# Kernel tuning notes

Hardware: AMD Instinct MI355X
Metric: run time of the kernel (lower is better)

The kernel has to match this reference:

```python
import math
import jax, jax.numpy as jnp
import numpy as np

B, T, D = 8, 2048, 256
N_TICKS, DT, P_MIN, P_MAX = 3, 1.0, 2.0, 4.0


def setup_inputs() -> dict:
    key = jax.random.key(0)
    ks = jax.random.split(key, 16)
    s = 1.0 / math.sqrt(D)
    w = lambda k: jax.random.normal(k, (D, D), jnp.float32) * s
    zb = jnp.zeros((D,), jnp.float32)
    return {
        "z": jax.random.normal(ks[0], (B, T, D), jnp.float32),
        "in_w": w(ks[1]), "in_b": zb,
        "ln_g": jnp.ones((D,), jnp.float32), "ln_b": zb,
        "q_w": w(ks[2]), "q_b": zb,
        "k_w": w(ks[3]), "k_b": zb,
        "v_w": w(ks[4]), "v_b": zb,
        "o_w": w(ks[5]), "o_b": zb,
        "log_tau": jnp.zeros((D,), jnp.float32),
        "p1_w": w(ks[6]), "p1_b": zb,
        "p2_w": w(ks[7]), "p2_b": zb,
    }


def _layernorm(x, g, b, eps=1e-5):
    mu = jnp.mean(x, axis=-1, keepdims=True)
    var = jnp.var(x, axis=-1, keepdims=True)
    return (x - mu) * jax.lax.rsqrt(var + eps) * g + b


def _lin(x, w, b):
    return x @ w.T + b


def reference(z, in_w, in_b, ln_g, ln_b, q_w, q_b, k_w, k_b, v_w, v_b,
              o_w, o_b, log_tau, p1_w, p1_b, p2_w, p2_b):
    tau = jnp.exp(log_tau)  # [d]
    inv_sqrt_d = 1.0 / math.sqrt(D)
    uniform = 1.0 / T
    pred_losses, eff_ps = [], []
    for _ in range(N_TICKS):
        h = _layernorm(_lin(z, in_w, in_b), ln_g, ln_b)
        Q, K, V = _lin(h, q_w, q_b), _lin(h, k_w, k_b), _lin(h, v_w, v_b)
        sim = jnp.einsum('btd,bsd->bts', Q, K) * inv_sqrt_d  # [B,T,T]
        attn = jax.nn.softmax(sim, axis=-1)
        row_max = jnp.max(attn, axis=-1)  # [B,T]
        conf = (jnp.mean(row_max, axis=-1) - uniform) / (1.0 - uniform + 1e-6)
        conf = jnp.clip(conf, 0.0, 1.0)  # [B]
        eff_p = P_MIN + (P_MAX - P_MIN) * conf
        eff_ps.append(jax.lax.stop_gradient(eff_p))
        attn_sharp = jax.nn.softmax(sim * eff_p[:, None, None], axis=-1)
        context = jnp.einsum('bts,bsd->btd', attn_sharp, V)
        target = _lin(context, o_w, o_b)
        z_pred = _lin(jax.nn.relu(_lin(z, p1_w, p1_b)), p2_w, p2_b)
        dz = (target - z) / (tau + 1e-6)
        z_next = z + DT * dz
        pred_losses.append(jnp.mean((z_pred - jax.lax.stop_gradient(z_next)) ** 2))
        z = z_next
    pred_loss_mean = jnp.mean(jnp.stack(pred_losses))
    eff_p_mean = jnp.mean(jnp.concatenate(eff_ps))
    return z, pred_loss_mean, eff_p_mean
```

## Files before the change

### kernel.cpp

```cpp
#include <hip/hip_runtime.h>
#include <math.h>

#define Bn 8
#define Tn 2048
#define Dn 256
#define NTICK 3
#define NROWS (Bn*Tn)
#define ABM 64
#define NBLKA (NROWS/ABM)
#define BS 64
#define GM 64
#define NBLKG (NROWS/GM)
#define WP 65536

typedef unsigned int u32;
typedef unsigned short u16;
typedef __attribute__((ext_vector_type(8))) short bf16x8;
typedef __attribute__((ext_vector_type(4))) float f32x4;
typedef __attribute__((ext_vector_type(16))) float f32x16;

__device__ __forceinline__ float bf2f(u32 u){
  union { u32 i; float f; } x; x.i = u << 16; return x.f;
}
__device__ __forceinline__ u16 f2bf(float f){
  union { float f; u32 i; } x; x.f = f;
  u32 r = (x.i + 0x7fffu + ((x.i >> 16) & 1u)) >> 16;
  return (u16)r;
}
__device__ __forceinline__ void gld_lds16(const u16* gsrc, u16* ldst){
  __builtin_amdgcn_global_load_lds(
      (const __attribute__((address_space(1))) u32*)(const void*)gsrc,
      (__attribute__((address_space(3))) u32*)(void*)ldst, 16, 0, 0);
}

__device__ __forceinline__ void stage_A(const u16* __restrict__ A, int row0, char* smem){
  const int tid = threadIdx.x, lane = tid & 63, w = tid >> 6;
  #pragma unroll
  for (int r=0;r<8;++r){
    int s = w*16 + 2*r + (lane>>5);
    int slot = (lane & 31) ^ (s & 7);
    gld_lds16(A + (size_t)(row0 + s)*Dn + slot*8, (u16*)(smem + (w*16 + 2*r)*512));
  }
}
__device__ __forceinline__ void load_frags(const char* smem, bf16x8* af){
  const int tid = threadIdx.x, lane = tid & 63, w = tid >> 6;
  const int l7 = lane & 7, g = (lane >> 4) & 3, q15 = lane & 15;
  const char* ab = smem + (w*16 + q15)*512;
  #pragma unroll
  for (int kk=0;kk<8;++kk) af[kk] = *(const bf16x8*)(ab + 16*((4*kk+g)^l7));
}
__device__ __forceinline__ void stage_Wchunk(const u16* __restrict__ W, int c, char* wbuf){
  const int tid = threadIdx.x, lane = tid & 63, w = tid >> 6;
  #pragma unroll
  for (int r=0;r<2;++r){
    int rl = w*4 + 2*r + (lane>>5);
    int slot = (lane & 31) ^ (rl & 7);
    gld_lds16(W + (size_t)(c*16 + rl)*Dn + slot*8, (u16*)(wbuf + (w*4 + 2*r)*512));
  }
}
__device__ __forceinline__ void load_wfrags(const char* wbuf, bf16x8* wf){
  const int lane = threadIdx.x & 63;
  const int l7 = lane & 7, g = (lane >> 4) & 3, q15 = lane & 15;
  const char* wb_ = wbuf + q15*512;
  #pragma unroll
  for (int kk=0;kk<8;++kk) wf[kk] = *(const bf16x8*)(wb_ + 16*((4*kk+g)^l7));
}
__device__ __forceinline__ void zero_acc(f32x4* acc){
  #pragma unroll
  for (int nt=0;nt<16;++nt) acc[nt] = (f32x4){0.f,0.f,0.f,0.f};
}
#define CHUNK_STEP(c, NC, PLANE_OF, IDX_OF)                                    \
  asm volatile("s_waitcnt lgkmcnt(0)" ::: "memory");                           \
  if ((c) < (NC)-2) { asm volatile("s_waitcnt vmcnt(2)" ::: "memory"); }       \
  else              { asm volatile("s_waitcnt vmcnt(0)" ::: "memory"); }       \
  __builtin_amdgcn_sched_barrier(0);                                           \
  __builtin_amdgcn_s_barrier();                                                \
  if ((c)+3 < (NC)) stage_Wchunk(PLANE_OF((c)+3), IDX_OF((c)+3), ring + (((c)+3)&3)*8192);

__global__ void k_prep(const float* __restrict__ s0, const float* __restrict__ s1,
                       const float* __restrict__ s2, const float* __restrict__ s3,
                       const float* __restrict__ s4, const float* __restrict__ s5,
                       const float* __restrict__ s6, u16* __restrict__ dst){
  int y = blockIdx.y;
  const float* s = (y==0)?s0:(y==1)?s1:(y==2)?s2:(y==3)?s3:(y==4)?s4:(y==5)?s5:s6;
  int i = (blockIdx.x*256 + threadIdx.x)*4;
  float4 v = *(const float4*)(s + i);
  u16 h0=f2bf(v.x), h1=f2bf(v.y), h2=f2bf(v.z), h3=f2bf(v.w);
  uint2 hi, lo;
  hi.x = (u32)h0 | ((u32)h1 << 16);
  hi.y = (u32)h2 | ((u32)h3 << 16);
  lo.x = (u32)f2bf(v.x - bf2f(h0)) | ((u32)f2bf(v.y - bf2f(h1)) << 16);
  lo.y = (u32)f2bf(v.z - bf2f(h2)) | ((u32)f2bf(v.w - bf2f(h3)) << 16);
  *(uint2*)(dst + (size_t)y*WP + i) = hi;
  *(uint2*)(dst + (size_t)(7+y)*WP + i) = lo;
}

__global__ void k_split(const float* __restrict__ s, u16* __restrict__ dh, u16* __restrict__ dl,
                        float* __restrict__ stats){
  if (blockIdx.x == 0 && threadIdx.x < 64) stats[threadIdx.x] = 0.f;
  int i = (blockIdx.x*256 + threadIdx.x)*4;
  float4 v = *(const float4*)(s + i);
  u16 h0=f2bf(v.x), h1=f2bf(v.y), h2=f2bf(v.z), h3=f2bf(v.w);
  uint2 hi, lo;
  hi.x = (u32)h0 | ((u32)h1 << 16);
  hi.y = (u32)h2 | ((u32)h3 << 16);
  lo.x = (u32)f2bf(v.x - bf2f(h0)) | ((u32)f2bf(v.y - bf2f(h1)) << 16);
  lo.y = (u32)f2bf(v.z - bf2f(h2)) | ((u32)f2bf(v.w - bf2f(h3)) << 16);
  *(uint2*)(dh + i) = hi;
  *(uint2*)(dl + i) = lo;
}

__global__ __launch_bounds__(256) void k_gemm_ln(
    const u16* __restrict__ Ahi, const u16* __restrict__ Alo,
    const u16* __restrict__ Whi, const u16* __restrict__ Wlo,
    const float* __restrict__ bias, const float* __restrict__ gamma, const float* __restrict__ beta,
    u16* __restrict__ h)
{
  __shared__ __align__(16) char smem[65536];
  char* ring = smem;
  f32x4 acc[16];
  const int row0 = blockIdx.x * GM;
  stage_A(Ahi, row0, smem);
  stage_A(Alo, row0, smem + 32768);
  asm volatile("s_waitcnt vmcnt(0)" ::: "memory");
  __builtin_amdgcn_sched_barrier(0);
  bf16x8 afh[8], afl[8];
  load_frags(smem, afh);
  load_frags(smem + 32768, afl);
  asm volatile("s_waitcnt lgkmcnt(0)" ::: "memory");
  __builtin_amdgcn_sched_barrier(0);
  __builtin_amdgcn_s_barrier();
  zero_acc(acc);
  #define LN_PL(i) ((i) < 16 ? Whi : Wlo)
  #define LN_IX(i) ((i) & 15)
  stage_Wchunk(LN_PL(0), LN_IX(0), ring + 0*8192);
  stage_Wchunk(LN_PL(1), LN_IX(1), ring + 1*8192);
  stage_Wchunk(LN_PL(2), LN_IX(2), ring + 2*8192);
  asm volatile("s_waitcnt vmcnt(4)" ::: "memory");
  __builtin_amdgcn_sched_barrier(0);
  __builtin_amdgcn_s_barrier();
  for (int c=0; c<32; ++c){
    bf16x8 wf[8];
    load_wfrags(ring + (c&3)*8192, wf);
    int nt = c & 15;
    if (c < 16){
      #pragma unroll
      for (int kk=0;kk<8;++kk)
        acc[nt] = __builtin_amdgcn_mfma_f32_16x16x32_bf16(afh[kk], wf[kk], acc[nt], 0,0,0);
      #pragma unroll
      for (int kk=0;kk<8;++kk)
        acc[nt] = __builtin_amdgcn_mfma_f32_16x16x32_bf16(afl[kk], wf[kk], acc[nt], 0,0,0);
    } else {
      #pragma unroll
      for (int kk=0;kk<8;++kk)
        acc[nt] = __builtin_amdgcn_mfma_f32_16x16x32_bf16(afh[kk], wf[kk], acc[nt], 0,0,0);
    }
    CHUNK_STEP(c, 32, LN_PL, LN_IX)
  }
  const int tid = threadIdx.x, lane = tid & 63, w = tid >> 6;
  const int g4 = lane >> 4, q15 = lane & 15;
  float bcol[16], gcol[16], becol[16];
  #pragma unroll
  for (int nt=0;nt<16;++nt){
    int col = nt*16 + q15;
    bcol[nt] = bias[col]; gcol[nt] = gamma[col]; becol[nt] = beta[col];
  }
  float mu[4], rstd[4];
  #pragma unroll
  for (int j=0;j<4;++j){
    float s=0.f, q=0.f;
    #pragma unroll
    for (int nt=0;nt<16;++nt){ float v = acc[nt][j] + bcol[nt]; s += v; q += v*v; }
    #pragma unroll
    for (int off=1; off<16; off<<=1){ s += __shfl_xor(s,off); q += __shfl_xor(q,off); }
    float m = s*(1.f/Dn);
    mu[j] = m; rstd[j] = rsqrtf(q*(1.f/Dn) - m*m + 1e-5f);
  }
  const size_t rbase = (size_t)(row0 + w*16 + g4*4);
  #pragma unroll
  for (int nt=0;nt<16;++nt){
    #pragma unroll
    for (int j=0;j<4;++j){
      float v = (acc[nt][j] + bcol[nt] - mu[j])*rstd[j]*gcol[nt] + becol[nt];
      h[(rbase+j)*Dn + nt*16 + q15] = f2bf(v);
    }
  }
}

__global__ __launch_bounds__(256) void k_gemm_qkv(
    const u16* __restrict__ h, const u16* __restrict__ wbf,
    const float* __restrict__ qb, const float* __restrict__ kb, const float* __restrict__ vb,
    u16* __restrict__ Qo, u16* __restrict__ Ko, u16* __restrict__ Vo)
{
  const u16 *Whi, *Wlo; const float* bias; u16* out;
  if (blockIdx.y == 0){ Whi = wbf + 1*WP; Wlo = wbf + 8*WP;  bias = qb; out = Qo; }
  else if (blockIdx.y == 1){ Whi = wbf + 2*WP; Wlo = wbf + 9*WP;  bias = kb; out = Ko; }
  else { Whi = wbf + 3*WP; Wlo = wbf + 10*WP; bias = vb; out = Vo; }
  __shared__ __align__(16) char smem[65536];
  char* ring = smem + 32768;
  f32x4 acc[16];
  const int row0 = blockIdx.x * GM;
  stage_A(h, row0, smem);
  #define QK_PL(i) ((i) < 16 ? Whi : Wlo)
  #define QK_IX(i) ((i) & 15)
  stage_Wchunk(QK_PL(0), QK_IX(0), ring + 0*8192);
  stage_Wchunk(QK_PL(1), QK_IX(1), ring + 1*8192);
  stage_Wchunk(QK_PL(2), QK_IX(2), ring + 2*8192);
  asm volatile("s_waitcnt vmcnt(4)" ::: "memory");
  __builtin_amdgcn_sched_barrier(0);
  bf16x8 af[8];
  load_frags(smem, af);
  zero_acc(acc);
  __builtin_amdgcn_s_barrier();
  for (int c=0; c<32; ++c){
    bf16x8 wf[8];
    load_wfrags(ring + (c&3)*8192, wf);
    int nt = c & 15;
    #pragma unroll
    for (int kk=0;kk<8;++kk)
      acc[nt] = __builtin_amdgcn_mfma_f32_16x16x32_bf16(af[kk], wf[kk], acc[nt], 0,0,0);
    CHUNK_STEP(c, 32, QK_PL, QK_IX)
  }
  const int tid = threadIdx.x, lane = tid & 63, w = tid >> 6;
  const int g4 = lane >> 4, q15 = lane & 15;
  const size_t rbase = (size_t)(row0 + w*16 + g4*4);
  #pragma unroll
  for (int nt=0;nt<16;++nt){
    float bc = bias[nt*16 + q15];
    #pragma unroll
    for (int j=0;j<4;++j)
      out[(rbase+j)*Dn + nt*16 + q15] = f2bf(acc[nt][j] + bc);
  }
}

__global__ __launch_bounds__(256) void k_gemm_update(
    const u16* __restrict__ Chi, const u16* __restrict__ Clo,
    const u16* __restrict__ Whi, const u16* __restrict__ Wlo,
    const float* __restrict__ ob,
    const u16* __restrict__ zhi_old, const u16* __restrict__ zlo_old,
    const float* __restrict__ log_tau,
    u16* __restrict__ zhi_new, u16* __restrict__ zlo_new,
    float* __restrict__ zout)
{
  __shared__ __align__(16) char smem[65536];
  char* ring = smem;
  f32x4 acc[16];
  const int row0 = blockIdx.x * GM;
  stage_A(Chi, row0, smem);
  stage_A(Clo, row0, smem + 32768);
  asm volatile("s_waitcnt vmcnt(0)" ::: "memory");
  __builtin_amdgcn_sched_barrier(0);
  bf16x8 afh[8], afl[8];
  load_frags(smem, afh);
  load_frags(smem + 32768, afl);
  asm volatile("s_waitcnt lgkmcnt(0)" ::: "memory");
  __builtin_amdgcn_sched_barrier(0);
  __builtin_amdgcn_s_barrier();
  zero_acc(acc);
  stage_Wchunk(LN_PL(0), LN_IX(0), ring + 0*8192);
  stage_Wchunk(LN_PL(1), LN_IX(1), ring + 1*8192);
  stage_Wchunk(LN_PL(2), LN_IX(2), ring + 2*8192);
  asm volatile("s_waitcnt vmcnt(4)" ::: "memory");
  __builtin_amdgcn_sched_barrier(0);
  __builtin_amdgcn_s_barrier();
  for (int c=0; c<32; ++c){
    bf16x8 wf[8];
    load_wfrags(ring + (c&3)*8192, wf);
    int nt = c & 15;
    if (c < 16){
      #pragma unroll
      for (int kk=0;kk<8;++kk)
        acc[nt] = __builtin_amdgcn_mfma_f32_16x16x32_bf16(afh[kk], wf[kk], acc[nt], 0,0,0);
      #pragma unroll
      for (int kk=0;kk<8;++kk)
        acc[nt] = __builtin_amdgcn_mfma_f32_16x16x32_bf16(afl[kk], wf[kk], acc[nt], 0,0,0);
    } else {
      #pragma unroll
      for (int kk=0;kk<8;++kk)
        acc[nt] = __builtin_amdgcn_mfma_f32_16x16x32_bf16(afh[kk], wf[kk], acc[nt], 0,0,0);
    }
    CHUNK_STEP(c, 32, LN_PL, LN_IX)
  }
  const int tid = threadIdx.x, lane = tid & 63, w = tid >> 6;
  const int g4 = lane >> 4, q15 = lane & 15;
  const size_t rbase = (size_t)(row0 + w*16 + g4*4);
  #pragma unroll
  for (int nt=0;nt<16;++nt){
    int col = nt*16 + q15;
    float bc = ob[col];
    float invt = 1.f/(expf(log_tau[col]) + 1e-6f);
    #pragma unroll
    for (int j=0;j<4;++j){
      size_t idx = (rbase+j)*Dn + col;
      float zo = bf2f(zhi_old[idx]) + bf2f(zlo_old[idx]);
      float zn = zo + (acc[nt][j] + bc - zo)*invt;
      u16 zh = f2bf(zn);
      zhi_new[idx] = zh;
      zlo_new[idx] = f2bf(zn - bf2f(zh));
      if (zout) zout[idx] = zn;
    }
  }
}

__global__ __launch_bounds__(256) void k_gemm_relu(
    const u16* __restrict__ A, const u16* __restrict__ Wb, const float* __restrict__ bias,
    u16* __restrict__ t1)
{
  __shared__ __align__(16) char smem[65536];
  char* ring = smem + 32768;
  f32x4 acc[16];
  const int row0 = blockIdx.x * GM;
  stage_A(A, row0, smem);
  #define W1_PL(i) (Wb)
  #define W1_IX(i) (i)
  stage_Wchunk(Wb, 0, ring + 0*8192);
  stage_Wchunk(Wb, 1, ring + 1*8192);
  stage_Wchunk(Wb, 2, ring + 2*8192);
  asm volatile("s_waitcnt vmcnt(4)" ::: "memory");
  __builtin_amdgcn_sched_barrier(0);
  bf16x8 af[8];
  load_frags(smem, af);
  zero_acc(acc);
  __builtin_amdgcn_s_barrier();
  for (int c=0; c<16; ++c){
    bf16x8 wf[8];
    load_wfrags(ring + (c&3)*8192, wf);
    #pragma unroll
    for (int kk=0;kk<8;++kk)
      acc[c] = __builtin_amdgcn_mfma_f32_16x16x32_bf16(af[kk], wf[kk], acc[c], 0,0,0);
    CHUNK_STEP(c, 16, W1_PL, W1_IX)
  }
  const int tid = threadIdx.x, lane = tid & 63, w = tid >> 6;
  const int g4 = lane >> 4, q15 = lane & 15;
  const size_t rbase = (size_t)(row0 + w*16 + g4*4);
  #pragma unroll
  for (int nt=0;nt<16;++nt){
    float bc = bias[nt*16 + q15];
    #pragma unroll
    for (int j=0;j<4;++j)
      t1[(rbase+j)*Dn + nt*16 + q15] = f2bf(fmaxf(acc[nt][j] + bc, 0.f));
  }
}

__global__ __launch_bounds__(256) void k_gemm_loss(
    const u16* __restrict__ t1, const u16* __restrict__ Wb, const float* __restrict__ bias,
    const u16* __restrict__ zhi_new, const u16* __restrict__ zlo_new,
    float* __restrict__ loss_acc)
{
  __shared__ __align__(16) char smem[65536];
  __shared__ float red[4];
  char* ring = smem + 32768;
  f32x4 acc[16];
  const int row0 = blockIdx.x * GM;
  stage_A(t1, row0, smem);
  stage_Wchunk(Wb, 0, ring + 0*8192);
  stage_Wchunk(Wb, 1, ring + 1*8192);
  stage_Wchunk(Wb, 2, ring + 2*8192);
  asm volatile("s_waitcnt vmcnt(4)" ::: "memory");
  __builtin_amdgcn_sched_barrier(0);
  bf16x8 af[8];
  load_frags(smem, af);
  zero_acc(acc);
  __builtin_amdgcn_s_barrier();
  for (int c=0; c<16; ++c){
    bf16x8 wf[8];
    load_wfrags(ring + (c&3)*8192, wf);
    #pragma unroll
    for (int kk=0;kk<8;++kk)
      acc[c] = __builtin_amdgcn_mfma_f32_16x16x32_bf16(af[kk], wf[kk], acc[c], 0,0,0);
    CHUNK_STEP(c, 16, W1_PL, W1_IX)
  }
  const int tid = threadIdx.x, lane = tid & 63, w = tid >> 6;
  const int g4 = lane >> 4, q15 = lane & 15;
  const size_t rbase = (size_t)(row0 + w*16 + g4*4);
  float lsum = 0.f;
  #pragma unroll
  for (int nt=0;nt<16;++nt){
    float bc = bias[nt*16 + q15];
    #pragma unroll
    for (int j=0;j<4;++j){
      size_t idx = (rbase+j)*Dn + nt*16 + q15;
      float zn = bf2f(zhi_new[idx]) + bf2f(zlo_new[idx]);
      float dn = acc[nt][j] + bc - zn;
      lsum += dn*dn;
    }
  }
  #pragma unroll
  for (int off=1; off<64; off<<=1) lsum += __shfl_xor(lsum, off);
  if (lane == 0) red[w] = lsum;
  __syncthreads();
  if (tid == 0) atomicAdd(loss_acc, red[0]+red[1]+red[2]+red[3]);
}

__global__ __launch_bounds__(256) void k_passA(
    const u16* __restrict__ Qg, const u16* __restrict__ Kg,
    float* __restrict__ conf_b, float* __restrict__ mrow)
{
  __shared__ __align__(16) char smem[65536];
  const int tid = threadIdx.x;
  const int lane = tid & 63, w = tid >> 6;
  const int l31 = lane & 31, hi5 = lane >> 5;
  const int qh = w >> 1, sh = w & 1;
  const int row0 = blockIdx.x * ABM;
  const int b = row0 >> 11;
  const size_t kbase = (size_t)b * Tn * Dn;

  #pragma unroll
  for (int r=0;r<8;++r){
    int s = w*16 + 2*r + (lane>>5);
    int slot = (lane & 31) ^ (s & 7);
    gld_lds16(Qg + (size_t)(row0 + s)*Dn + slot*8, (u16*)(smem + (w*16 + 2*r)*512));
  }
  asm volatile("s_waitcnt vmcnt(0)" ::: "memory");
  __builtin_amdgcn_sched_barrier(0);
  __builtin_amdgcn_s_barrier();
  bf16x8 qf[16];
  {
    const char* qb = smem + (qh*32 + l31)*512;
    const int r7 = l31 & 7;
    #pragma unroll
    for (int t=0;t<16;++t) qf[t] = *(const bf16x8*)(qb + 16*((2*t+hi5)^r7));
  }
  asm volatile("s_waitcnt lgkmcnt(0)" ::: "memory");
  __builtin_amdgcn_sched_barrier(0);
  __builtin_amdgcn_s_barrier();
  #pragma unroll
  for (int r=0;r<8;++r){
    int s = w*16 + 2*r + (lane>>5);
    int slot = (lane & 31) ^ (s & 7);
    gld_lds16(Kg + kbase + (size_t)(s)*Dn + slot*8, (u16*)(smem + 32768 + (w*16 + 2*r)*512));
  }
  #pragma unroll
  for (int r=0;r<8;++r){
    int s = w*16 + 2*r + (lane>>5);
    int slot = (lane & 31) ^ (s & 7);
    gld_lds16(Kg + kbase + (size_t)(BS + s)*Dn + slot*8, (u16*)(smem + (w*16 + 2*r)*512));
  }
  asm volatile("s_waitcnt vmcnt(8)" ::: "memory");
  __builtin_amdgcn_sched_barrier(0);
  __builtin_amdgcn_s_barrier();

  float m_run = -INFINITY, l_run = 0.f;
  const int sr7 = l31 & 7;
  int cur = 1;
  for (int tile=0; tile<Tn/BS; ++tile){
    const char* kb = smem + cur*32768 + (sh*32 + l31)*512;
    f32x16 sc = (f32x16)(0.f);
    #pragma unroll
    for (int t=0;t<16;++t){
      bf16x8 kf = *(const bf16x8*)(kb + 16*((2*t+hi5)^sr7));
      sc = __builtin_amdgcn_mfma_f32_32x32x16_bf16(kf, qf[t], sc, 0,0,0);
    }
    float vmax = -INFINITY;
    float vals[16];
    #pragma unroll
    for (int i=0;i<16;++i){ float v = sc[i]*0.0625f; vals[i]=v; vmax=fmaxf(vmax,v); }
    vmax = fmaxf(vmax, __shfl_xor(vmax,32));
    float mnew = fmaxf(m_run, vmax);
    float corr = __expf(m_run - mnew);
    float esum = 0.f;
    #pragma unroll
    for (int i=0;i<16;++i) esum += __expf(vals[i]-mnew);
    esum += __shfl_xor(esum,32);
    l_run = l_run*corr + esum;
    m_run = mnew;

    asm volatile("s_waitcnt vmcnt(0)" ::: "memory");
    __builtin_amdgcn_sched_barrier(0);
    __builtin_amdgcn_s_barrier();
    if (tile < Tn/BS - 2){
      #pragma unroll
      for (int r=0;r<8;++r){
        int s = w*16 + 2*r + (lane>>5);
        int slot = (lane & 31) ^ (s & 7);
        gld_lds16(Kg + kbase + (size_t)((tile+2)*BS + s)*Dn + slot*8,
                  (u16*)(smem + cur*32768 + (w*16 + 2*r)*512));
      }
    }
    cur ^= 1;
  }
  __syncthreads();
  if (sh == 1 && lane < 32){
    float2 ml; ml.x = m_run; ml.y = l_run;
    *(float2*)(smem + (qh*32 + l31)*8) = ml;
  }
  __syncthreads();
  if (sh == 0){
    float2 o = *(const float2*)(smem + (qh*32 + l31)*8);
    float m2 = fmaxf(m_run, o.x);
    float lm = l_run*__expf(m_run - m2) + o.y*__expf(o.x - m2);
    if (lane < 32) mrow[row0 + qh*32 + l31] = m2;
    float r1 = 1.f/lm;
    #pragma unroll
    for (int off=1; off<64; off<<=1) r1 += __shfl_xor(r1, off);
    if (lane==0) atomicAdd(conf_b + b, r1*0.5f);
  }
}

#define KB0 0
#define KB1 32768
#define VT0 65536
#define VT1 98304
#define PST 131072
__global__ __launch_bounds__(512) void k_passB(
    const u16* __restrict__ Qg, const u16* __restrict__ Kg, const u16* __restrict__ Vg,
    const float* __restrict__ conf_sum, const float* __restrict__ mrow,
    u16* __restrict__ Chi, u16* __restrict__ Clo)
{
  __shared__ __align__(16) char smem[139264];
  const int tid = threadIdx.x;
  const int lane = tid & 63, w = tid >> 6;
  const int qg = w & 3, hs = w >> 2;
  const int l7 = lane & 7, g = (lane >> 4) & 3, q15 = lane & 15;
  const int row0 = blockIdx.x * ABM;
  const int b = row0 >> 11;
  const size_t kbase = (size_t)b * Tn * Dn;
  float mean_rm = conf_sum[b] * (1.f/Tn);
  float uniform = 1.f/Tn;
  float conf = fminf(fmaxf((mean_rm - uniform)/(1.f - uniform + 1e-6f), 0.f), 1.f);
  const float scale = (2.f + 2.f*conf) * 0.0625f;
  const float mfix = mrow[row0 + qg*16 + q15] * scale * 16.f;
  const int tid2 = tid & 255;
  const int dblk = tid2 >> 3, sblk = tid2 & 7;
  uint4 vreg[8];
  const int NT = Tn/BS;

  if (hs == 0){
    #pragma unroll
    for (int r=0;r<8;++r){
      int s = w*16 + 2*r + (lane>>5);
      int slot = (lane & 31) ^ (s & 7);
      gld_lds16(Qg + (size_t)(row0 + s)*Dn + slot*8, (u16*)(smem + KB0 + (w*16 + 2*r)*512));
    }
  } else {
    const u16* vsrc = Vg + kbase + (size_t)(sblk*8)*Dn + dblk*8;
    #pragma unroll
    for (int si=0; si<8; ++si) vreg[si] = *(const uint4*)(vsrc + (size_t)si*Dn);
  }
  __syncthreads();
  bf16x8 qf[8];
  {
    const char* qb = smem + KB0 + (qg*16 + q15)*512;
    #pragma unroll
    for (int kk=0;kk<8;++kk) qf[kk] = *(const bf16x8*)(qb + 16*((4*kk+g)^l7));
  }
  __syncthreads();
  if (hs == 0){
    #pragma unroll
    for (int r=0;r<8;++r){
      int s = w*16 + 2*r + (lane>>5);
      int slot = (lane & 31) ^ (s & 7);
      gld_lds16(Kg + kbase + (size_t)(s)*Dn + slot*8, (u16*)(smem + KB0 + (w*16 + 2*r)*512));
    }
    #pragma unroll
    for (int r=0;r<8;++r){
      int s = w*16 + 2*r + (lane>>5);
      int slot = (lane & 31) ^ (s & 7);
      gld_lds16(Kg + kbase + (size_t)(BS + s)*Dn + slot*8, (u16*)(smem + KB1 + (w*16 + 2*r)*512));
    }
    asm volatile("s_waitcnt vmcnt(8)" ::: "memory");
    __builtin_amdgcn_sched_barrier(0);
  } else {
    const u32* rw = (const u32*)vreg;
    #pragma unroll
    for (int dl=0; dl<8; ++dl){
      int wi = dl >> 1;
      u32 sel = (dl & 1) ? 0x07060302u : 0x05040100u;
      uint4 o;
      o.x = __builtin_amdgcn_perm(rw[1*4+wi], rw[0*4+wi], sel);
      o.y = __builtin_amdgcn_perm(rw[3*4+wi], rw[2*4+wi], sel);
      o.z = __builtin_amdgcn_perm(rw[5*4+wi], rw[4*4+wi], sel);
      o.w = __builtin_amdgcn_perm(rw[7*4+wi], rw[6*4+wi], sel);
      int d = dblk*8 + dl;
      *(uint4*)(smem + VT0 + d*128 + 16*(sblk ^ dl)) = o;
    }
    asm volatile("s_waitcnt lgkmcnt(0)" ::: "memory");
    __builtin_amdgcn_sched_barrier(0);
  }
  __builtin_amdgcn_s_barrier();

  float l_run = 0.f;
  f32x4 oa[16];
  #pragma unroll
  for (int md=0;md<16;++md) oa[md] = (f32x4){0.f,0.f,0.f,0.f};

  char* pbase = smem + PST + w*1024 + q15*64;
  const int psw = q15 & 3;

  int cur = 0;
  for (int tile=0; tile<NT; ++tile){
    const char* kbuf = smem + (cur ? KB1 : KB0);
    const char* vbuf = smem + (cur ? VT1 : VT0);
    char* vbuf_n = (char*)smem + (cur ? VT0 : VT1);
    if (hs == 1 && tile < NT-1){
      const u16* vsrc = Vg + kbase + (size_t)((tile+1)*BS + sblk*8)*Dn + dblk*8;
      #pragma unroll
      for (int si=0; si<8; ++si) vreg[si] = *(const uint4*)(vsrc + (size_t)si*Dn);
    }
    f32x4 sc[2];
    sc[0] = (f32x4){0.f,0.f,0.f,0.f};
    sc[1] = (f32x4){0.f,0.f,0.f,0.f};
    #pragma unroll
    for (int kk=0;kk<8;++kk){
      #pragma unroll
      for (int msl=0;msl<2;++msl){
        int msg = 2*hs + msl;
        bf16x8 kf = *(const bf16x8*)(kbuf + (msg*16+q15)*512 + 16*((4*kk+g)^l7));
        sc[msl] = __builtin_amdgcn_mfma_f32_16x16x32_bf16(kf, qf[kk], sc[msl], 0,0,0);
      }
    }
    float vals[8];
    float esum = 0.f;
    #pragma unroll
    for (int msl=0;msl<2;++msl){
      #pragma unroll
      for (int j=0;j<4;++j){
        float p = __expf(sc[msl][j]*scale - mfix);
        vals[msl*4+j] = p; esum += p;
      }
    }
    esum += __shfl_xor(esum,16); esum += __shfl_xor(esum,32);
    l_run += esum;
    #pragma unroll
    for (int msl=0;msl<2;++msl){
      uint2 pw;
      pw.x = (u32)f2bf(vals[msl*4+0]) | ((u32)f2bf(vals[msl*4+1]) << 16);
      pw.y = (u32)f2bf(vals[msl*4+2]) | ((u32)f2bf(vals[msl*4+3]) << 16);
      int slot = (2*msl + (g>>1)) ^ psw;
      *(uint2*)(pbase + slot*16 + (g&1)*8) = pw;
    }
    asm volatile("s_waitcnt lgkmcnt(0)" ::: "memory");
    __builtin_amdgcn_sched_barrier(0);
    {
      bf16x8 pf = *(const bf16x8*)(pbase + ((g ^ psw)*16));
      #pragma unroll
      for (int md=0; md<16; ++md){
        bf16x8 vf = *(const bf16x8*)(vbuf + (md*16+q15)*128 + 16*((4*hs+g)^l7));
        oa[md] = __builtin_amdgcn_mfma_f32_16x16x32_bf16(vf, pf, oa[md], 0,0,0);
      }
    }
    if (hs == 1){
      if (tile < NT-1){
        asm volatile("s_waitcnt vmcnt(0)" ::: "memory");
        __builtin_amdgcn_sched_barrier(0);
        const u32* rw = (const u32*)vreg;
        #pragma unroll
        for (int dl=0; dl<8; ++dl){
          int wi = dl >> 1;
          u32 sel = (dl & 1) ? 0x07060302u : 0x05040100u;
          uint4 o;
          o.x = __builtin_amdgcn_perm(rw[1*4+wi], rw[0*4+wi], sel);
          o.y = __builtin_amdgcn_perm(rw[3*4+wi], rw[2*4+wi], sel);
          o.z = __builtin_amdgcn_perm(rw[5*4+wi], rw[4*4+wi], sel);
          o.w = __builtin_amdgcn_perm(rw[7*4+wi], rw[6*4+wi], sel);
          int d = dblk*8 + dl;
          *(uint4*)(vbuf_n + d*128 + 16*(sblk ^ dl)) = o;
        }
      }
      asm volatile("s_waitcnt lgkmcnt(0)" ::: "memory");
    } else {
      asm volatile("s_waitcnt vmcnt(0) lgkmcnt(0)" ::: "memory");
    }
    __builtin_amdgcn_sched_barrier(0);
    __builtin_amdgcn_s_barrier();
    if (hs == 0 && tile < NT-2){
      #pragma unroll
      for (int r=0;r<8;++r){
        int s = w*16 + 2*r + (lane>>5);
        int slot = (lane & 31) ^ (s & 7);
        gld_lds16(Kg + kbase + (size_t)((tile+2)*BS + s)*Dn + slot*8,
                  (u16*)(smem + (cur ? KB1 : KB0) + (w*16 + 2*r)*512));
      }
    }
    cur ^= 1;
  }
  __syncthreads();
  if (hs == 1){
    char* ob_ = smem + (qg*64 + lane)*256;
    #pragma unroll
    for (int md=0; md<16; ++md)
      *(f32x4*)(ob_ + (md ^ q15)*16) = oa[md];
    *(float*)(smem + VT0 + (qg*64 + lane)*4) = l_run;
  }
  __syncthreads();
  if (hs == 0){
    float lo_ = *(const float*)(smem + VT0 + (qg*64 + lane)*4);
    float inv = 1.f / (l_run + lo_);
    const char* ob_ = smem + (qg*64 + lane)*256;
    const size_t rr = (size_t)(row0 + qg*16 + q15)*Dn + g*4;
    #pragma unroll
    for (int md=0; md<16; ++md){
      f32x4 ob = *(const f32x4*)(ob_ + (md ^ q15)*16);
      float v0 = (oa[md][0] + ob[0])*inv;
      float v1 = (oa[md][1] + ob[1])*inv;
      float v2 = (oa[md][2] + ob[2])*inv;
      float v3 = (oa[md][3] + ob[3])*inv;
      uint2 hi, lo;
      u16 h0=f2bf(v0), h1=f2bf(v1), h2=f2bf(v2), h3=f2bf(v3);
      hi.x = (u32)h0 | ((u32)h1 << 16);
      hi.y = (u32)h2 | ((u32)h3 << 16);
      lo.x = (u32)f2bf(v0 - bf2f(h0)) | ((u32)f2bf(v1 - bf2f(h1)) << 16);
      lo.y = (u32)f2bf(v2 - bf2f(h2)) | ((u32)f2bf(v3 - bf2f(h3)) << 16);
      *(uint2*)(Chi + rr + md*16) = hi;
      *(uint2*)(Clo + rr + md*16) = lo;
    }
  }
}

__global__ void k_finalize(const float* __restrict__ loss3, const float* __restrict__ conf_sum,
                           float* __restrict__ out_scalars){
  if (threadIdx.x == 0){
    float ls = (loss3[0]+loss3[1]+loss3[2]) * (1.f/(3.f*NROWS*Dn));
    float es = 0.f;
    float uniform = 1.f/Tn;
    #pragma unroll
    for (int i=0;i<NTICK*Bn;++i){
      float mean_rm = conf_sum[i] * (1.f/Tn);
      float conf = fminf(fmaxf((mean_rm - uniform)/(1.f - uniform + 1e-6f), 0.f), 1.f);
      es += 2.f + 2.f*conf;
    }
    out_scalars[0] = ls;
    out_scalars[1] = es * (1.f/(NTICK*Bn));
  }
}

extern "C" void kernel_launch(void* const* d_in, const int* in_sizes, int n_in,
                              void* d_out, int out_size, void* d_ws, size_t ws_size,
                              hipStream_t stream) {
  (void)in_sizes; (void)n_in; (void)out_size; (void)ws_size;
  const float* z_in   = (const float*)d_in[0];
  const float* in_w   = (const float*)d_in[1];
  const float* in_b   = (const float*)d_in[2];
  const float* ln_g   = (const float*)d_in[3];
  const float* ln_b   = (const float*)d_in[4];
  const float* q_w    = (const float*)d_in[5];
  const float* q_b    = (const float*)d_in[6];
  const float* k_w    = (const float*)d_in[7];
  const float* k_b    = (const float*)d_in[8];
  const float* v_w    = (const float*)d_in[9];
  const float* v_b    = (const float*)d_in[10];
  const float* o_w    = (const float*)d_in[11];
  const float* o_b    = (const float*)d_in[12];
  const float* log_tau= (const float*)d_in[13];
  const float* p1_w   = (const float*)d_in[14];
  const float* p1_b   = (const float*)d_in[15];
  const float* p2_w   = (const float*)d_in[16];
  const float* p2_b   = (const float*)d_in[17];

  float* out = (float*)d_out;
  const size_t NE = (size_t)NROWS * Dn;

  u16*  zh0  = (u16*)d_ws;
  u16*  zl0  = zh0 + NE;
  u16*  zh1  = zl0 + NE;
  u16*  zl1  = zh1 + NE;
  u16*  hbuf = zl1 + NE;
  u16*  Qb   = hbuf + NE;
  u16*  Kb   = Qb + NE;
  u16*  Vb   = Kb + NE;
  u16*  Chi  = Vb + NE;
  u16*  Clo  = Chi + NE;
  u16*  t1b  = Clo + NE;
  u16*  wbf  = t1b + NE;
  float* stats = (float*)(wbf + 14*WP);
  float* conf_sum = stats;
  float* loss     = stats + 24;
  float* mrowb    = stats + 64;

  k_prep<<<dim3(64,7), 256, 0, stream>>>(in_w, q_w, k_w, v_w, o_w, p1_w, p2_w, wbf);
  k_split<<<4096, 256, 0, stream>>>(z_in, zh0, zl0, stats);

  u16* zh_list[2] = { zh0, zh1 };
  u16* zl_list[2] = { zl0, zl1 };

  for (int t = 0; t < NTICK; ++t){
    u16* zh_old = zh_list[t & 1];
    u16* zl_old = zl_list[t & 1];
    u16* zh_new = zh_list[(t+1) & 1];
    u16* zl_new = zl_list[(t+1) & 1];
    float* zout = (t == NTICK-1) ? out : nullptr;
    k_gemm_ln<<<NBLKG, 256, 0, stream>>>(zh_old, zl_old, wbf + 0*WP, wbf + 7*WP,
                                         in_b, ln_g, ln_b, hbuf);
    k_gemm_qkv<<<dim3(NBLKG,3), 256, 0, stream>>>(hbuf, wbf, q_b, k_b, v_b, Qb, Kb, Vb);
    k_passA<<<NBLKA, 256, 0, stream>>>(Qb, Kb, conf_sum + t*8, mrowb);
    k_passB<<<NBLKA, 512, 0, stream>>>(Qb, Kb, Vb, conf_sum + t*8, mrowb, Chi, Clo);
    k_gemm_update<<<NBLKG, 256, 0, stream>>>(Chi, Clo, wbf + 4*WP, wbf + 11*WP, o_b,
                                             zh_old, zl_old, log_tau, zh_new, zl_new, zout);
    k_gemm_relu<<<NBLKG, 256, 0, stream>>>(zh_old, wbf + 5*WP, p1_b, t1b);
    k_gemm_loss<<<NBLKG, 256, 0, stream>>>(t1b, wbf + 6*WP, p2_b, zh_new, zl_new, loss + t);
  }
  k_finalize<<<1, 64, 0, stream>>>(loss, conf_sum, out + NE);
}
```

Baseline: 742.9 us.

## Fuse input projection+LayerNorm with QKV projections in one kernel

Merges the in-projection/LayerNorm GEMM and the three QKV GEMMs into a single kernel. The normalized h tile now stays in swizzled shared memory instead of round-tripping through global memory, and one launch replaces two. Each block then runs Q, K and V serially through a single 128-chunk weight stream, where before they were spread over a 3x grid. This cuts parallelism from 768 to 256 blocks and lengthens each block's critical path.

Result: slower. 933.2 us (+25.6%).

```diff
diff --git a/kernel.cpp b/kernel.cpp
--- a/kernel.cpp
+++ b/kernel.cpp
@@ -110,16 +110,21 @@
   *(uint2*)(dl + i) = lo;
 }
 
-__global__ __launch_bounds__(256) void k_gemm_ln(
-    const u16* __restrict__ Ahi, const u16* __restrict__ Alo,
-    const u16* __restrict__ Whi, const u16* __restrict__ Wlo,
+#define FQ_PL(i) (wbf + (size_t)WP * (size_t)(((((i)>>4)&1)*7) + ((i)>>5)))
+#define FQ_IX(i) ((i) & 15)
+__global__ __launch_bounds__(256) void k_fused_lnqkv(
+    const u16* __restrict__ Ahi, const u16* __restrict__ Alo, const u16* __restrict__ wbf,
     const float* __restrict__ bias, const float* __restrict__ gamma, const float* __restrict__ beta,
-    u16* __restrict__ h)
+    const float* __restrict__ qb, const float* __restrict__ kb, const float* __restrict__ vb,
+    u16* __restrict__ Qo, u16* __restrict__ Ko, u16* __restrict__ Vo)
 {
   __shared__ __align__(16) char smem[65536];
   char* ring = smem;
   f32x4 acc[16];
   const int row0 = blockIdx.x * GM;
+  const int tid = threadIdx.x, lane = tid & 63, w = tid >> 6;
+  const int g4 = lane >> 4, q15 = lane & 15;
+
   stage_A(Ahi, row0, smem);
   stage_A(Alo, row0, smem + 32768);
   asm volatile("s_waitcnt vmcnt(0)" ::: "memory");
@@ -131,14 +136,13 @@
   __builtin_amdgcn_sched_barrier(0);
   __builtin_amdgcn_s_barrier();
   zero_acc(acc);
-  #define LN_PL(i) ((i) < 16 ? Whi : Wlo)
-  #define LN_IX(i) ((i) & 15)
-  stage_Wchunk(LN_PL(0), LN_IX(0), ring + 0*8192);
-  stage_Wchunk(LN_PL(1), LN_IX(1), ring + 1*8192);
-  stage_Wchunk(LN_PL(2), LN_IX(2), ring + 2*8192);
+  stage_Wchunk(FQ_PL(0), FQ_IX(0), ring + 0*8192);
+  stage_Wchunk(FQ_PL(1), FQ_IX(1), ring + 1*8192);
+  stage_Wchunk(FQ_PL(2), FQ_IX(2), ring + 2*8192);
   asm volatile("s_waitcnt vmcnt(4)" ::: "memory");
   __builtin_amdgcn_sched_barrier(0);
   __builtin_amdgcn_s_barrier();
+
   for (int c=0; c<32; ++c){
     bf16x8 wf[8];
     load_wfrags(ring + (c&3)*8192, wf);
@@ -155,81 +159,78 @@
       for (int kk=0;kk<8;++kk)
         acc[nt] = __builtin_amdgcn_mfma_f32_16x16x32_bf16(afh[kk], wf[kk], acc[nt], 0,0,0);
     }
-    CHUNK_STEP(c, 32, LN_PL, LN_IX)
-  }
-  const int tid = threadIdx.x, lane = tid & 63, w = tid >> 6;
-  const int g4 = lane >> 4, q15 = lane & 15;
-  float bcol[16], gcol[16], becol[16];
-  #pragma unroll
-  for (int nt=0;nt<16;++nt){
-    int col = nt*16 + q15;
-    bcol[nt] = bias[col]; gcol[nt] = gamma[col]; becol[nt] = beta[col];
-  }
-  float mu[4], rstd[4];
-  #pragma unroll
-  for (int j=0;j<4;++j){
-    float s=0.f, q=0.f;
-    #pragma unroll
-    for (int nt=0;nt<16;++nt){ float v = acc[nt][j] + bcol[nt]; s += v; q += v*v; }
-    #pragma unroll
-    for (int off=1; off<16; off<<=1){ s += __shfl_xor(s,off); q += __shfl_xor(q,off); }
-    float m = s*(1.f/Dn);
-    mu[j] = m; rstd[j] = rsqrtf(q*(1.f/Dn) - m*m + 1e-5f);
-  }
-  const size_t rbase = (size_t)(row0 + w*16 + g4*4);
-  #pragma unroll
-  for (int nt=0;nt<16;++nt){
+    CHUNK_STEP(c, 128, FQ_PL, FQ_IX)
+  }
+
+  {
+    float bcol[16], gcol[16], becol[16];
+    #pragma unroll
+    for (int nt=0;nt<16;++nt){
+      int col = nt*16 + q15;
+      bcol[nt] = bias[col]; gcol[nt] = gamma[col]; becol[nt] = beta[col];
+    }
+    float mu[4], rstd[4];
     #pragma unroll
     for (int j=0;j<4;++j){
-      float v = (acc[nt][j] + bcol[nt] - mu[j])*rstd[j]*gcol[nt] + becol[nt];
-      h[(rbase+j)*Dn + nt*16 + q15] = f2bf(v);
-    }
-  }
-}
-
-__global__ __launch_bounds__(256) void k_gemm_qkv(
-    const u16* __restrict__ h, const u16* __restrict__ wbf,
-    const float* __restrict__ qb, const float* __restrict__ kb, const float* __restrict__ vb,
-    u16* __restrict__ Qo, u16* __restrict__ Ko, u16* __restrict__ Vo)
-{
-  const u16 *Whi, *Wlo; const float* bias; u16* out;
-  if (blockIdx.y == 0){ Whi = wbf + 1*WP; Wlo = wbf + 8*WP;  bias = qb; out = Qo; }
-  else if (blockIdx.y == 1){ Whi = wbf + 2*WP; Wlo = wbf + 9*WP;  bias = kb; out = Ko; }
-  else { Whi = wbf + 3*WP; Wlo = wbf + 10*WP; bias = vb; out = Vo; }
-  __shared__ __align__(16) char smem[65536];
-  char* ring = smem + 32768;
-  f32x4 acc[16];
-  const int row0 = blockIdx.x * GM;
-  stage_A(h, row0, smem);
-  #define QK_PL(i) ((i) < 16 ? Whi : Wlo)
-  #define QK_IX(i) ((i) & 15)
-  stage_Wchunk(QK_PL(0), QK_IX(0), ring + 0*8192);
-  stage_Wchunk(QK_PL(1), QK_IX(1), ring + 1*8192);
-  stage_Wchunk(QK_PL(2), QK_IX(2), ring + 2*8192);
-  asm volatile("s_waitcnt vmcnt(4)" ::: "memory");
+      float s=0.f, q=0.f;
+      #pragma unroll
+      for (int nt=0;nt<16;++nt){ float v = acc[nt][j] + bcol[nt]; s += v; q += v*v; }
+      #pragma unroll
+      for (int off=1; off<16; off<<=1){ s += __shfl_xor(s,off); q += __shfl_xor(q,off); }
+      float m = s*(1.f/Dn);
+      mu[j] = m; rstd[j] = rsqrtf(q*(1.f/Dn) - m*m + 1e-5f);
+    }
+    u16* hb = (u16*)(smem + 32768);
+    #pragma unroll
+    for (int nt=0;nt<16;++nt){
+      #pragma unroll
+      for (int j=0;j<4;++j){
+        float v = (acc[nt][j] + bcol[nt] - mu[j])*rstd[j]*gcol[nt] + becol[nt];
+        int r = w*16 + g4*4 + j;
+        int phys = (nt*2 + (q15>>3)) ^ (r & 7);
+        hb[r*256 + phys*8 + (q15&7)] = f2bf(v);
+      }
+    }
+  }
+  asm volatile("s_waitcnt lgkmcnt(0)" ::: "memory");
   __builtin_amdgcn_sched_barrier(0);
   bf16x8 af[8];
-  load_frags(smem, af);
+  load_frags(smem + 32768, af);
   zero_acc(acc);
-  __builtin_amdgcn_s_barrier();
-  for (int c=0; c<32; ++c){
+
+  for (int c=32; c<128; ++c){
     bf16x8 wf[8];
     load_wfrags(ring + (c&3)*8192, wf);
     int nt = c & 15;
     #pragma unroll
     for (int kk=0;kk<8;++kk)
       acc[nt] = __builtin_amdgcn_mfma_f32_16x16x32_bf16(af[kk], wf[kk], acc[nt], 0,0,0);
-    CHUNK_STEP(c, 32, QK_PL, QK_IX)
-  }
-  const int tid = threadIdx.x, lane = tid & 63, w = tid >> 6;
-  const int g4 = lane >> 4, q15 = lane & 15;
-  const size_t rbase = (size_t)(row0 + w*16 + g4*4);
-  #pragma unroll
-  for (int nt=0;nt<16;++nt){
-    float bc = bias[nt*16 + q15];
-    #pragma unroll
-    for (int j=0;j<4;++j)
-      out[(rbase+j)*Dn + nt*16 + q15] = f2bf(acc[nt][j] + bc);
+    CHUNK_STEP(c, 128, FQ_PL, FQ_IX)
+    if (c == 63 || c == 95){
+      const float* bp = (c == 63) ? qb : kb;
+      u16* op = (c == 63) ? Qo : Ko;
+      const size_t rbase = (size_t)(row0 + w*16 + g4*4);
+      #pragma unroll
+      for (int nt2=0;nt2<16;++nt2){
+        float bc = bp[nt2*16 + q15];
+        #pragma unroll
+        for (int j=0;j<4;++j)
+          op[(rbase+j)*Dn + nt2*16 + q15] = f2bf(acc[nt2][j] + bc);
+      }
+      zero_acc(acc);
+      asm volatile("s_waitcnt vmcnt(0)" ::: "memory");
+      __builtin_amdgcn_sched_barrier(0);
+    }
+  }
+  {
+    const size_t rbase = (size_t)(row0 + w*16 + g4*4);
+    #pragma unroll
+    for (int nt=0;nt<16;++nt){
+      float bc = vb[nt*16 + q15];
+      #pragma unroll
+      for (int j=0;j<4;++j)
+        Vo[(rbase+j)*Dn + nt*16 + q15] = f2bf(acc[nt][j] + bc);
+    }
   }
 }
 
@@ -257,6 +258,8 @@
   __builtin_amdgcn_sched_barrier(0);
   __builtin_amdgcn_s_barrier();
   zero_acc(acc);
+  #define LN_PL(i) ((i) < 16 ? Whi : Wlo)
+  #define LN_IX(i) ((i) & 15)
   stage_Wchunk(LN_PL(0), LN_IX(0), ring + 0*8192);
   stage_Wchunk(LN_PL(1), LN_IX(1), ring + 1*8192);
   stage_Wchunk(LN_PL(2), LN_IX(2), ring + 2*8192);
@@ -779,9 +782,8 @@
     u16* zh_new = zh_list[(t+1) & 1];
     u16* zl_new = zl_list[(t+1) & 1];
     float* zout = (t == NTICK-1) ? out : nullptr;
-    k_gemm_ln<<<NBLKG, 256, 0, stream>>>(zh_old, zl_old, wbf + 0*WP, wbf + 7*WP,
-                                         in_b, ln_g, ln_b, hbuf);
-    k_gemm_qkv<<<dim3(NBLKG,3), 256, 0, stream>>>(hbuf, wbf, q_b, k_b, v_b, Qb, Kb, Vb);
+    k_fused_lnqkv<<<NBLKG, 256, 0, stream>>>(zh_old, zl_old, wbf,
+                                             in_b, ln_g, ln_b, q_b, k_b, v_b, Qb, Kb, Vb);
     k_passA<<<NBLKA, 256, 0, stream>>>(Qb, Kb, conf_sum + t*8, mrowb);
     k_passB<<<NBLKA, 512, 0, stream>>>(Qb, Kb, Vb, conf_sum + t*8, mrowb, Chi, Clo);
     k_gemm_update<<<NBLKG, 256, 0, stream>>>(Chi, Clo, wbf + 4*WP, wbf + 11*WP, o_b,
```

## Fuse predictor MLP GEMMs into one kernel keeping hidden activations in LDS

Applied to the files above, without the earlier changes.

Merges the ReLU GEMM and the loss GEMM of the predictor MLP into a single kernel. The bias-plus-ReLU hidden tile is written in bf16 to shared memory with a swizzled layout, then reloaded as A fragments for the second GEMM. This removes the global round trip of the intermediate t1 buffer and one launch per tick. In exchange the kernel runs longer and restages W2 into the shared ring without an explicit barrier, so correctness depends on how the chunk pipeline synchronises its waves.

Measured after the change: 748.4 us. About the same (+0.7%).

```diff
diff --git a/kernel.cpp b/kernel.cpp
--- a/kernel.cpp
+++ b/kernel.cpp
@@ -302,48 +302,9 @@
   }
 }
 
-__global__ __launch_bounds__(256) void k_gemm_relu(
-    const u16* __restrict__ A, const u16* __restrict__ Wb, const float* __restrict__ bias,
-    u16* __restrict__ t1)
-{
-  __shared__ __align__(16) char smem[65536];
-  char* ring = smem + 32768;
-  f32x4 acc[16];
-  const int row0 = blockIdx.x * GM;
-  stage_A(A, row0, smem);
-  #define W1_PL(i) (Wb)
-  #define W1_IX(i) (i)
-  stage_Wchunk(Wb, 0, ring + 0*8192);
-  stage_Wchunk(Wb, 1, ring + 1*8192);
-  stage_Wchunk(Wb, 2, ring + 2*8192);
-  asm volatile("s_waitcnt vmcnt(4)" ::: "memory");
-  __builtin_amdgcn_sched_barrier(0);
-  bf16x8 af[8];
-  load_frags(smem, af);
-  zero_acc(acc);
-  __builtin_amdgcn_s_barrier();
-  for (int c=0; c<16; ++c){
-    bf16x8 wf[8];
-    load_wfrags(ring + (c&3)*8192, wf);
-    #pragma unroll
-    for (int kk=0;kk<8;++kk)
-      acc[c] = __builtin_amdgcn_mfma_f32_16x16x32_bf16(af[kk], wf[kk], acc[c], 0,0,0);
-    CHUNK_STEP(c, 16, W1_PL, W1_IX)
-  }
-  const int tid = threadIdx.x, lane = tid & 63, w = tid >> 6;
-  const int g4 = lane >> 4, q15 = lane & 15;
-  const size_t rbase = (size_t)(row0 + w*16 + g4*4);
-  #pragma unroll
-  for (int nt=0;nt<16;++nt){
-    float bc = bias[nt*16 + q15];
-    #pragma unroll
-    for (int j=0;j<4;++j)
-      t1[(rbase+j)*Dn + nt*16 + q15] = f2bf(fmaxf(acc[nt][j] + bc, 0.f));
-  }
-}
-
-__global__ __launch_bounds__(256) void k_gemm_loss(
-    const u16* __restrict__ t1, const u16* __restrict__ Wb, const float* __restrict__ bias,
+__global__ __launch_bounds__(256) void k_gemm_mlp(
+    const u16* __restrict__ A, const u16* __restrict__ W1, const float* __restrict__ b1,
+    const u16* __restrict__ W2, const float* __restrict__ b2,
     const u16* __restrict__ zhi_new, const u16* __restrict__ zlo_new,
     float* __restrict__ loss_acc)
 {
@@ -352,10 +313,14 @@
   char* ring = smem + 32768;
   f32x4 acc[16];
   const int row0 = blockIdx.x * GM;
-  stage_A(t1, row0, smem);
-  stage_Wchunk(Wb, 0, ring + 0*8192);
-  stage_Wchunk(Wb, 1, ring + 1*8192);
-  stage_Wchunk(Wb, 2, ring + 2*8192);
+  const int tid = threadIdx.x, lane = tid & 63, w = tid >> 6;
+  const int g4 = lane >> 4, q15 = lane & 15;
+  stage_A(A, row0, smem);
+  #define M1_PL(i) (W1)
+  #define M1_IX(i) (i)
+  stage_Wchunk(W1, 0, ring + 0*8192);
+  stage_Wchunk(W1, 1, ring + 1*8192);
+  stage_Wchunk(W1, 2, ring + 2*8192);
   asm volatile("s_waitcnt vmcnt(4)" ::: "memory");
   __builtin_amdgcn_sched_barrier(0);
   bf16x8 af[8];
@@ -368,15 +333,46 @@
     #pragma unroll
     for (int kk=0;kk<8;++kk)
       acc[c] = __builtin_amdgcn_mfma_f32_16x16x32_bf16(af[kk], wf[kk], acc[c], 0,0,0);
-    CHUNK_STEP(c, 16, W1_PL, W1_IX)
-  }
-  const int tid = threadIdx.x, lane = tid & 63, w = tid >> 6;
-  const int g4 = lane >> 4, q15 = lane & 15;
+    CHUNK_STEP(c, 16, M1_PL, M1_IX)
+  }
+  {
+    u16* hb = (u16*)smem;
+    #pragma unroll
+    for (int nt=0;nt<16;++nt){
+      float bc = b1[nt*16 + q15];
+      #pragma unroll
+      for (int j=0;j<4;++j){
+        float v = fmaxf(acc[nt][j] + bc, 0.f);
+        int r = w*16 + g4*4 + j;
+        int phys = (nt*2 + (q15>>3)) ^ (r & 7);
+        hb[r*256 + phys*8 + (q15&7)] = f2bf(v);
+      }
+    }
+  }
+  asm volatile("s_waitcnt lgkmcnt(0)" ::: "memory");
+  __builtin_amdgcn_sched_barrier(0);
+  load_frags(smem, af);
+  zero_acc(acc);
+  #define M2_PL(i) (W2)
+  stage_Wchunk(W2, 0, ring + 0*8192);
+  stage_Wchunk(W2, 1, ring + 1*8192);
+  stage_Wchunk(W2, 2, ring + 2*8192);
+  asm volatile("s_waitcnt vmcnt(4)" ::: "memory");
+  __builtin_amdgcn_sched_barrier(0);
+  __builtin_amdgcn_s_barrier();
+  for (int c=0; c<16; ++c){
+    bf16x8 wf[8];
+    load_wfrags(ring + (c&3)*8192, wf);
+    #pragma unroll
+    for (int kk=0;kk<8;++kk)
+      acc[c] = __builtin_amdgcn_mfma_f32_16x16x32_bf16(af[kk], wf[kk], acc[c], 0,0,0);
+    CHUNK_STEP(c, 16, M2_PL, M1_IX)
+  }
   const size_t rbase = (size_t)(row0 + w*16 + g4*4);
   float lsum = 0.f;
   #pragma unroll
   for (int nt=0;nt<16;++nt){
-    float bc = bias[nt*16 + q15];
+    float bc = b2[nt*16 + q15];
     #pragma unroll
     for (int j=0;j<4;++j){
       size_t idx = (rbase+j)*Dn + nt*16 + q15;
@@ -786,8 +782,8 @@
     k_passB<<<NBLKA, 512, 0, stream>>>(Qb, Kb, Vb, conf_sum + t*8, mrowb, Chi, Clo);
     k_gemm_update<<<NBLKG, 256, 0, stream>>>(Chi, Clo, wbf + 4*WP, wbf + 11*WP, o_b,
                                              zh_old, zl_old, log_tau, zh_new, zl_new, zout);
-    k_gemm_relu<<<NBLKG, 256, 0, stream>>>(zh_old, wbf + 5*WP, p1_b, t1b);
-    k_gemm_loss<<<NBLKG, 256, 0, stream>>>(t1b, wbf + 6*WP, p2_b, zh_new, zl_new, loss + t);
+    k_gemm_mlp<<<NBLKG, 256, 0, stream>>>(zh_old, wbf + 5*WP, p1_b, wbf + 6*WP, p2_b,
+                                          zh_new, zl_new, loss + t);
   }
   k_finalize<<<1, 64, 0, stream>>>(loss, conf_sum, out + NE);
 }
```
